# Kernel tuning notes

Hardware: AMD Instinct MI355X
Metric: run time of the kernel (lower is better)

Reference implementation:

```python
import jax, jax.numpy as jnp
import numpy as np

HIDDEN = 1024
Q_OUT = 2048
KV_OUT = 1024
HEAD_DIM = 128
N_Q = Q_OUT // HEAD_DIM      # 16
N_KV = KV_OUT // HEAD_DIM    # 8
EPS = 1e-6
ROPE_BASE = 10000.0


def _rms_norm(x, w, eps=EPS):
    # normalize over last dim (head_dim)
    ms = jnp.mean(x * x, axis=-1, keepdims=True)
    return x * jax.lax.rsqrt(ms + eps) * w


def _rope_cos_sin(t, dim=HEAD_DIM, base=ROPE_BASE):
    inv_freq = 1.0 / (base ** (jnp.arange(0, dim, 2, dtype=jnp.float32) / dim))
    pos = jnp.arange(t, dtype=jnp.float32)
    freqs = pos[:, None] * inv_freq[None, :]          # (T, D/2)
    emb = jnp.concatenate([freqs, freqs], axis=-1)    # (T, D)
    return jnp.cos(emb), jnp.sin(emb)


def _rotate_half(x):
    d = x.shape[-1] // 2
    return jnp.concatenate([-x[..., d:], x[..., :d]], axis=-1)


def setup_inputs() -> dict:
    key = jax.random.key(0)
    ks = jax.random.split(key, 7)
    def lin(k, fan_in, fan_out):
        # nn.Linear default init: U(-1/sqrt(fan_in), 1/sqrt(fan_in)); stored as (in, out) for x @ W
        bound = 1.0 / np.sqrt(fan_in)
        return jax.random.uniform(k, (fan_in, fan_out), jnp.float32, -bound, bound)
    return {
        "x": jax.random.normal(ks[0], (2, 2048, HIDDEN), jnp.float32),
        "Wq": lin(ks[1], HIDDEN, Q_OUT),
        "Wk": lin(ks[2], HIDDEN, KV_OUT),
        "Wv": lin(ks[3], HIDDEN, KV_OUT),
        "Wo": lin(ks[4], Q_OUT, HIDDEN),
        "q_norm_w": jnp.ones((HEAD_DIM,), jnp.float32),
        "k_norm_w": jnp.ones((HEAD_DIM,), jnp.float32),
    }


def reference(x, Wq, Wk, Wv, Wo, q_norm_w, k_norm_w):
    b, t, _ = x.shape
    # QKV projections, shaped to (B, H, T, D)
    q = (x @ Wq).reshape(b, t, N_Q, HEAD_DIM).transpose(0, 2, 1, 3)
    k = (x @ Wk).reshape(b, t, N_KV, HEAD_DIM).transpose(0, 2, 1, 3)
    v = (x @ Wv).reshape(b, t, N_KV, HEAD_DIM).transpose(0, 2, 1, 3)
    # per-head RMSNorm on q/k
    q = _rms_norm(q, q_norm_w)
    k = _rms_norm(k, k_norm_w)
    # RoPE (positions 0..T-1)
    cos, sin = _rope_cos_sin(t)                        # (T, D)
    cos = cos[None, None]; sin = sin[None, None]       # (1,1,T,D)
    q = q * cos + _rotate_half(q) * sin
    k = k * cos + _rotate_half(k) * sin
    # GQA: repeat_interleave kv heads to match q heads
    rep = N_Q // N_KV
    k_r = jnp.repeat(k, rep, axis=1)                   # (B, Hq, T, D)
    v_r = jnp.repeat(v, rep, axis=1)
    # causal attention
    scores = jnp.einsum('bhqd,bhkd->bhqk', q, k_r) / jnp.sqrt(jnp.asarray(HEAD_DIM, x.dtype))
    causal = jnp.triu(jnp.full((t, t), -jnp.inf, dtype=scores.dtype), k=1)[None, None]
    attn = jax.nn.softmax(scores + causal, axis=-1)
    out = jnp.einsum('bhqk,bhkd->bhqd', attn, v_r)     # (B, Hq, T, D)
    out = out.transpose(0, 2, 1, 3).reshape(b, t, Q_OUT)
    return out @ Wo
```

## Files before the change

kernel.cpp:

```cpp
#include <hip/hip_runtime.h>
#include <math.h>

typedef __attribute__((ext_vector_type(8))) short short8;
typedef __attribute__((ext_vector_type(4))) float f32x4;
typedef __attribute__((ext_vector_type(4))) unsigned int uint4v;

#define HIDDEN 1024
#define QOUT 2048
#define KVOUT 1024
#define HD 128
#define TSEQ 2048

__device__ __forceinline__ float bf2f(unsigned short h) {
    union { unsigned int u; float f; } x; x.u = ((unsigned int)h) << 16; return x.f;
}
__device__ __forceinline__ unsigned short f2bf(float f) {
    union { float f; unsigned int u; } x; x.f = f;
    unsigned int r = (x.u + 0x7fffu + ((x.u >> 16) & 1u)) >> 16;
    return (unsigned short)r;
}
__device__ __forceinline__ unsigned int pk2bf(float lo, float hi) {
    return (unsigned int)f2bf(lo) | ((unsigned int)f2bf(hi) << 16);
}

__device__ __forceinline__ void glds16(const unsigned short* g, unsigned short* l) {
    __builtin_amdgcn_global_load_lds(
        (const __attribute__((address_space(1))) unsigned int*)g,
        (__attribute__((address_space(3))) unsigned int*)l, 16, 0, 0);
}

__global__ __launch_bounds__(256) void prep(const float* __restrict__ x,
                                            const float* __restrict__ Wq,
                                            const float* __restrict__ Wk,
                                            const float* __restrict__ Wv,
                                            const float* __restrict__ Wo,
                                            unsigned short* __restrict__ xb,
                                            unsigned short* __restrict__ Wt,
                                            unsigned short* __restrict__ Wot) {
    int bid = blockIdx.x;
    int tid = threadIdx.x;
    if (bid < 4096) {
        int i = bid * 256 + tid;
        float4 v = *(const float4*)(x + (size_t)i * 4);
        unsigned short o[4] = {f2bf(v.x), f2bf(v.y), f2bf(v.z), f2bf(v.w)};
        *(unsigned long long*)(xb + (size_t)i * 4) = *(unsigned long long*)o;
        return;
    }
    bid -= 4096;
    const float* W; unsigned short* D; int K, N;
    if (bid < 512)       { W = Wq; D = Wt;                          K = 1024; N = 2048; }
    else if (bid < 768)  { bid -= 512;  W = Wk; D = Wt + (size_t)2048 * 1024; K = 1024; N = 1024; }
    else if (bid < 1024) { bid -= 768;  W = Wv; D = Wt + (size_t)3072 * 1024; K = 1024; N = 1024; }
    else                 { bid -= 1024; W = Wo; D = Wot;                      K = 2048; N = 1024; }
    __shared__ __attribute__((aligned(16))) unsigned short Ls[64 * 72];
    int ntiles = N >> 6;
    int kt = bid / ntiles, nt = bid - kt * ntiles;
    int k0 = kt * 64, n0 = nt * 64;
    for (int t = 0; t < 4; t++) {
        int idx = tid + t * 256;
        int r = idx >> 4, seg = idx & 15;
        float4 v = *(const float4*)(W + (size_t)(k0 + r) * N + n0 + seg * 4);
        int c = seg * 4;
        Ls[(c + 0) * 72 + r] = f2bf(v.x);
        Ls[(c + 1) * 72 + r] = f2bf(v.y);
        Ls[(c + 2) * 72 + r] = f2bf(v.z);
        Ls[(c + 3) * 72 + r] = f2bf(v.w);
    }
    __syncthreads();
    for (int t = 0; t < 2; t++) {
        int idx = tid + t * 256;
        int rr = idx >> 3, seg = idx & 7;
        uint4v v = *(const uint4v*)(Ls + rr * 72 + seg * 8);
        *(uint4v*)(D + (size_t)(n0 + rr) * K + k0 + seg * 8) = v;
    }
}

template <int OUT_BF16, int BN>
__global__ __launch_bounds__(256) void gemm_bt(const unsigned short* __restrict__ A,
                                               const unsigned short* __restrict__ Bt,
                                               void* __restrict__ Cout,
                                               int M, int N, int K) {
    constexpr int MT = (BN == 128) ? 4 : 2;
    __shared__ __attribute__((aligned(16))) unsigned short As[2][128 * 32];
    __shared__ __attribute__((aligned(16))) unsigned short Bs[2][BN * 32];
    const int tid = threadIdx.x;
    const int lane = tid & 63;
    const int warp = tid >> 6;
    const int ln = lane & 15;
    const int quad = lane >> 4;
    const int wm = (BN == 128) ? (warp >> 1) : warp;
    const int wn = (BN == 128) ? (warp & 1) : 0;
    const int m0 = blockIdx.y * 128;
    const int n0 = blockIdx.x * BN;

    const int srow = lane >> 2;
    const int schunk = (lane & 3) ^ (srow & 3);
    const unsigned short* Ag = A + (size_t)(m0 + warp * 16 + srow) * K + schunk * 8;
    const unsigned short* Bg = Bt + (size_t)(n0 + warp * 16 + srow) * K + schunk * 8;

    f32x4 acc[MT][4];
#pragma unroll
    for (int i = 0; i < MT; i++)
#pragma unroll
        for (int j = 0; j < 4; j++) acc[i][j] = (f32x4){0.f, 0.f, 0.f, 0.f};

    auto stage = [&](int k0, int bi) {
        glds16(Ag + k0, As[bi] + warp * 16 * 32);
        glds16(Ag + (size_t)64 * K + k0, As[bi] + warp * 16 * 32 + 64 * 32);
        glds16(Bg + k0, Bs[bi] + warp * 16 * 32);
        if (BN == 128) glds16(Bg + (size_t)64 * K + k0, Bs[bi] + warp * 16 * 32 + 64 * 32);
    };

    const int rq = quad ^ (ln & 3);
    const int KI = K >> 5;
    stage(0, 0);
    for (int it = 0; it < KI; it++) {
        __syncthreads();
        if (it + 1 < KI) stage((it + 1) << 5, (it + 1) & 1);
        const unsigned short* Ab = As[it & 1];
        const unsigned short* Bb = Bs[it & 1];
        short8 af[MT], bf[4];
#pragma unroll
        for (int mt = 0; mt < MT; mt++)
            af[mt] = *(const short8*)(Ab + (wm * (MT * 16) + mt * 16 + ln) * 32 + rq * 8);
#pragma unroll
        for (int nt = 0; nt < 4; nt++)
            bf[nt] = *(const short8*)(Bb + (wn * 64 + nt * 16 + ln) * 32 + rq * 8);
#pragma unroll
        for (int mt = 0; mt < MT; mt++)
#pragma unroll
            for (int nt = 0; nt < 4; nt++)
                acc[mt][nt] = __builtin_amdgcn_mfma_f32_16x16x32_bf16(bf[nt], af[mt], acc[mt][nt], 0, 0, 0);
    }
#pragma unroll
    for (int mt = 0; mt < MT; mt++) {
        int row = m0 + wm * (MT * 16) + mt * 16 + ln;
#pragma unroll
        for (int nt = 0; nt < 4; nt++) {
            int colb = n0 + wn * 64 + nt * 16 + quad * 4;
            if (OUT_BF16) {
                unsigned long long pk =
                    (unsigned long long)pk2bf(acc[mt][nt][0], acc[mt][nt][1]) |
                    ((unsigned long long)pk2bf(acc[mt][nt][2], acc[mt][nt][3]) << 32);
                *(unsigned long long*)((unsigned short*)Cout + (size_t)row * N + colb) = pk;
            } else {
                *(f32x4*)((float*)Cout + (size_t)row * N + colb) = acc[mt][nt];
            }
        }
    }
}

__global__ __launch_bounds__(256) void nrvt(const unsigned short* __restrict__ QKV,
                                            const float* __restrict__ qw,
                                            const float* __restrict__ kw,
                                            unsigned short* __restrict__ Q,
                                            unsigned short* __restrict__ Kb,
                                            unsigned short* __restrict__ Vt) {
    if (blockIdx.x < 24576) {
        int warp = threadIdx.x >> 6;
        int lane = threadIdx.x & 63;
        int gid = blockIdx.x * 4 + warp;
        int tok = gid / 24;
        int slot = gid - tok * 24;
        int b = tok >> 11, t = tok & 2047;
        const float* w;
        unsigned short* dst;
        int col0;
        if (slot < 16) {
            col0 = slot * HD;
            dst = Q + ((size_t)(b * 16 + slot) * TSEQ + t) * HD;
            w = qw;
        } else {
            int hk = slot - 16;
            col0 = QOUT + hk * HD;
            dst = Kb + ((size_t)(b * 8 + hk) * TSEQ + t) * HD;
            w = kw;
        }
        const unsigned short* row = QKV + (size_t)tok * 4096 + col0;
        float e0 = bf2f(row[lane]), e1 = bf2f(row[lane + 64]);
        float ss = e0 * e0 + e1 * e1;
        for (int off = 1; off < 64; off <<= 1) ss += __shfl_xor(ss, off);
        float rr = rsqrtf(ss * (1.0f / 128.0f) + 1e-6f);
        float n0 = e0 * rr * w[lane];
        float n1 = e1 * rr * w[lane + 64];
        float invf = __builtin_exp2f(-(float)lane * 0.20762050593045951f);
        float ang = (float)t * invf;
        float sf, cf;
        __sincosf(ang, &sf, &cf);
        dst[lane] = f2bf(n0 * cf - n1 * sf);
        dst[lane + 64] = f2bf(n1 * cf + n0 * sf);
        return;
    }
    __shared__ __attribute__((aligned(16))) unsigned short Ls[128 * 72];
    int bid = blockIdx.x - 24576;
    int tt = bid & 31, hk = (bid >> 5) & 7, b = bid >> 8;
    int t0 = tt * 64;
    int tid = threadIdx.x;
    const unsigned short* base = QKV + (size_t)(b * 2048 + t0) * 4096 + 3072 + hk * 128;
    for (int i = 0; i < 4; i++) {
        int idx = tid + i * 256;
        int r = idx >> 4, seg = idx & 15;
        uint4v v = *(const uint4v*)(base + (size_t)r * 4096 + seg * 8);
        unsigned short* pv = (unsigned short*)&v;
        int d = seg * 8;
        for (int jj = 0; jj < 8; jj++) Ls[(d + jj) * 72 + r] = pv[jj];
    }
    __syncthreads();
    unsigned short* out = Vt + (size_t)(b * 8 + hk) * 128 * 2048;
    for (int i = 0; i < 4; i++) {
        int idx = tid + i * 256;
        int d = idx >> 3, seg = idx & 7;
        uint4v v = *(const uint4v*)(Ls + d * 72 + seg * 8);
        *(uint4v*)(out + (size_t)d * 2048 + t0 + seg * 8) = v;
    }
}

__global__ __launch_bounds__(256, 2) void attn(const unsigned short* __restrict__ Q,
                                               const unsigned short* __restrict__ Kg,
                                               const unsigned short* __restrict__ Vt,
                                               unsigned short* __restrict__ Og) {
    __shared__ __attribute__((aligned(16))) unsigned short Ks[2][64 * 128];
    __shared__ __attribute__((aligned(16))) unsigned short Vs[2][128 * 64];
    __shared__ __attribute__((aligned(16))) unsigned short Ps[4][16 * 72];
    const int p = blockIdx.x;
    const int bh = blockIdx.y;
    const int b = bh >> 4, h = bh & 15, hk = h >> 1;
    const int tid = threadIdx.x;
    const int warp = tid >> 6, lane = tid & 63, ln = lane & 15, quad = lane >> 4;
    const int strip[2] = { p * 64 + warp * 16, (31 - p) * 64 + warp * 16 };
    const int jdiag[2] = { p, 31 - p };

    const unsigned short* Kbase = Kg + (size_t)(b * 8 + hk) * TSEQ * HD;
    const unsigned short* Vbase = Vt + (size_t)(b * 8 + hk) * HD * TSEQ;
    const unsigned short* Qh = Q + (size_t)(b * 16 + h) * TSEQ * HD;

    short8 qf[2][4];
#pragma unroll
    for (int st = 0; st < 2; st++)
#pragma unroll
        for (int kt = 0; kt < 4; kt++)
            qf[st][kt] = *(const short8*)(Qh + (size_t)(strip[st] + ln) * HD + kt * 32 + quad * 8);

    f32x4 o[2][8];
#pragma unroll
    for (int st = 0; st < 2; st++)
#pragma unroll
        for (int ot = 0; ot < 8; ot++) o[st][ot] = (f32x4){0.f, 0.f, 0.f, 0.f};
    float m_[2] = {-1e30f, -1e30f}, l_[2] = {0.f, 0.f};

    const int kr = lane >> 4;
    const int kc = lane & 15;
    const int vr = lane >> 3;
    const int vc = lane & 7;

    auto stage_kv = [&](int jt, int bi) {
        const int j0s = jt * 64;
        unsigned short* KsB = Ks[bi];
        unsigned short* VsB = Vs[bi];
#pragma unroll
        for (int c = 0; c < 4; c++) {
            int row = warp * 16 + c * 4 + kr;
            glds16(Kbase + (size_t)(j0s + row) * HD + ((kc ^ (row & 15)) * 8),
                   KsB + (warp * 16 + c * 4) * 128);
        }
#pragma unroll
        for (int c = 0; c < 4; c++) {
            int d = warp * 32 + c * 8 + vr;
            glds16(Vbase + (size_t)d * TSEQ + j0s + ((vc ^ (d & 7)) * 8),
                   VsB + (warp * 32 + c * 8) * 64);
        }
    };

    const float kscale = 0.12750580997495268f;
    const int nT = 32 - p;
    stage_kv(0, 0);
    for (int j = 0; j < nT; j++) {
        __syncthreads();
        if (j + 1 < nT) stage_kv(j + 1, (j + 1) & 1);
        const unsigned short* KsC = Ks[j & 1];
        const unsigned short* VsC = Vs[j & 1];
        const bool act0 = (j <= jdiag[0]);
        f32x4 s[2][4];
#pragma unroll
        for (int kb = 0; kb < 4; kb++) {
            s[0][kb] = (f32x4){0.f, 0.f, 0.f, 0.f};
            s[1][kb] = (f32x4){0.f, 0.f, 0.f, 0.f};
        }
#pragma unroll
        for (int kt = 0; kt < 4; kt++) {
            short8 kf[4];
#pragma unroll
            for (int kb = 0; kb < 4; kb++)
                kf[kb] = *(const short8*)(KsC + (kb * 16 + ln) * 128 + (((kt * 4 + quad) ^ ln) * 8));
#pragma unroll
            for (int kb = 0; kb < 4; kb++)
                s[1][kb] = __builtin_amdgcn_mfma_f32_16x16x32_bf16(kf[kb], qf[1][kt], s[1][kb], 0, 0, 0);
            if (act0)
#pragma unroll
                for (int kb = 0; kb < 4; kb++)
                    s[0][kb] = __builtin_amdgcn_mfma_f32_16x16x32_bf16(kf[kb], qf[0][kt], s[0][kb], 0, 0, 0);
        }
        short8 pf[2][2];
        float al[2] = {1.f, 1.f};
#pragma unroll
        for (int st = 0; st < 2; st++) {
            if (st == 0 && !act0) continue;
            float mx = -1e30f;
            if (j == jdiag[st]) {
                const int qloc = warp * 16 + ln;
#pragma unroll
                for (int kb = 0; kb < 4; kb++)
#pragma unroll
                    for (int r = 0; r < 4; r++) {
                        int kvloc = kb * 16 + quad * 4 + r;
                        float v = s[st][kb][r] * kscale;
                        v = (kvloc > qloc) ? -1e30f : v;
                        s[st][kb][r] = v;
                        mx = fmaxf(mx, v);
                    }
            } else {
#pragma unroll
                for (int kb = 0; kb < 4; kb++)
#pragma unroll
                    for (int r = 0; r < 4; r++) {
                        float v = s[st][kb][r] * kscale;
                        s[st][kb][r] = v;
                        mx = fmaxf(mx, v);
                    }
            }
            mx = fmaxf(mx, __shfl_xor(mx, 16));
            mx = fmaxf(mx, __shfl_xor(mx, 32));
            float mn = fmaxf(m_[st], mx);
            al[st] = __builtin_exp2f(m_[st] - mn);
            float sum = 0.f;
#pragma unroll
            for (int kb = 0; kb < 4; kb++)
#pragma unroll
                for (int r = 0; r < 4; r++) {
                    float pv = __builtin_exp2f(s[st][kb][r] - mn);
                    s[st][kb][r] = pv;
                    sum += pv;
                }
            sum += __shfl_xor(sum, 16);
            sum += __shfl_xor(sum, 32);
            m_[st] = mn;
            l_[st] = l_[st] * al[st] + sum;
#pragma unroll
            for (int kb = 0; kb < 4; kb++) {
                unsigned long long pk =
                    (unsigned long long)pk2bf(s[st][kb][0], s[st][kb][1]) |
                    ((unsigned long long)pk2bf(s[st][kb][2], s[st][kb][3]) << 32);
                *(unsigned long long*)(&Ps[warp][ln * 72 + kb * 16 + quad * 4]) = pk;
            }
            pf[st][0] = *(const short8*)(&Ps[warp][ln * 72 + quad * 8]);
            pf[st][1] = *(const short8*)(&Ps[warp][ln * 72 + 32 + quad * 8]);
        }
        if (act0 && __any(al[0] != 1.0f))
#pragma unroll
            for (int ot = 0; ot < 8; ot++)
#pragma unroll
                for (int r = 0; r < 4; r++) o[0][ot][r] *= al[0];
        if (__any(al[1] != 1.0f))
#pragma unroll
            for (int ot = 0; ot < 8; ot++)
#pragma unroll
                for (int r = 0; r < 4; r++) o[1][ot][r] *= al[1];
#pragma unroll
        for (int ot = 0; ot < 8; ot++) {
            short8 vf0 = *(const short8*)(VsC + (ot * 16 + ln) * 64 + ((quad ^ (ln & 7)) * 8));
            short8 vf1 = *(const short8*)(VsC + (ot * 16 + ln) * 64 + (((4 + quad) ^ (ln & 7)) * 8));
            o[1][ot] = __builtin_amdgcn_mfma_f32_16x16x32_bf16(vf0, pf[1][0], o[1][ot], 0, 0, 0);
            o[1][ot] = __builtin_amdgcn_mfma_f32_16x16x32_bf16(vf1, pf[1][1], o[1][ot], 0, 0, 0);
            if (act0) {
                o[0][ot] = __builtin_amdgcn_mfma_f32_16x16x32_bf16(vf0, pf[0][0], o[0][ot], 0, 0, 0);
                o[0][ot] = __builtin_amdgcn_mfma_f32_16x16x32_bf16(vf1, pf[0][1], o[0][ot], 0, 0, 0);
            }
        }
    }
#pragma unroll
    for (int st = 0; st < 2; st++) {
        float inv = 1.0f / l_[st];
        size_t rowoff = ((size_t)(b * TSEQ + strip[st] + ln)) * QOUT + h * 128 + quad * 4;
#pragma unroll
        for (int ot = 0; ot < 8; ot++) {
            unsigned long long pk =
                (unsigned long long)pk2bf(o[st][ot][0] * inv, o[st][ot][1] * inv) |
                ((unsigned long long)pk2bf(o[st][ot][2] * inv, o[st][ot][3] * inv) << 32);
            *(unsigned long long*)(Og + rowoff + ot * 16) = pk;
        }
    }
}

extern "C" void kernel_launch(void* const* d_in, const int* in_sizes, int n_in,
                              void* d_out, int out_size, void* d_ws, size_t ws_size,
                              hipStream_t stream) {
    (void)in_sizes; (void)n_in; (void)out_size;
    const float* x  = (const float*)d_in[0];
    const float* Wq = (const float*)d_in[1];
    const float* Wk = (const float*)d_in[2];
    const float* Wv = (const float*)d_in[3];
    const float* Wo = (const float*)d_in[4];
    const float* qw = (const float*)d_in[5];
    const float* kw = (const float*)d_in[6];

    char* ws = (char*)d_ws;
    const size_t MB = 1024 * 1024;
    unsigned short* Wt   = (unsigned short*)(ws);
    unsigned short* Wot  = (unsigned short*)(ws + 8 * MB);
    unsigned short* QKVb = (unsigned short*)(ws + 12 * MB);
    unsigned short* xb   = (unsigned short*)(ws + 44 * MB);
    unsigned short* Qb   = (unsigned short*)(ws + 52 * MB);
    unsigned short* Kb   = (unsigned short*)(ws + 68 * MB);
    unsigned short* Vtb  = (unsigned short*)(ws + 76 * MB);
    unsigned short* Ob   = (unsigned short*)(ws + 84 * MB);
    if (ws_size < 100 * MB) return;

    prep<<<dim3(5632), 256, 0, stream>>>(x, Wq, Wk, Wv, Wo, xb, Wt, Wot);
    gemm_bt<1, 128><<<dim3(32, 32), 256, 0, stream>>>(xb, Wt, QKVb, 4096, 4096, 1024);
    nrvt<<<dim3(25088), 256, 0, stream>>>(QKVb, qw, kw, Qb, Kb, Vtb);
    attn<<<dim3(16, 32), 256, 0, stream>>>(Qb, Kb, Vtb, Ob);
    gemm_bt<0, 64><<<dim3(16, 32), 256, 0, stream>>>(Ob, Wot, (float*)d_out, 4096, 1024, 2048);
}
```

Before: 286.2 us.

## Split paired-strip attention blocks into one strip per block with higher occupancy

The attention kernel no longer pairs a short and a long causal query strip in one block. It now launches one block per 64-row strip, twice as many blocks, with the longest strips scheduled first. The double-buffered K/V staging becomes a single buffer loaded between two barriers, the P-tile LDS round trip becomes cross-lane shuffles, and launch bounds rise to 4 blocks per CU. This trades explicit load/compute overlap within a block for more parallelism, higher occupancy and less register and LDS use, which risks exposing global-load latency and adding barrier cost.

Result: slower. 325.1 us (+13.6%).

```diff
diff --git a/kernel.cpp b/kernel.cpp
--- a/kernel.cpp
+++ b/kernel.cpp
@@ -10,6 +10,8 @@
 #define KVOUT 1024
 #define HD 128
 #define TSEQ 2048
+
+union U8 { uint4v u; short8 s; };
 
 __device__ __forceinline__ float bf2f(unsigned short h) {
     union { unsigned int u; float f; } x; x.u = ((unsigned int)h) << 16; return x.f;
@@ -215,179 +217,151 @@
     }
 }
 
-__global__ __launch_bounds__(256, 2) void attn(const unsigned short* __restrict__ Q,
+__global__ __launch_bounds__(256, 4) void attn(const unsigned short* __restrict__ Q,
                                                const unsigned short* __restrict__ Kg,
                                                const unsigned short* __restrict__ Vt,
                                                unsigned short* __restrict__ Og) {
-    __shared__ __attribute__((aligned(16))) unsigned short Ks[2][64 * 128];
-    __shared__ __attribute__((aligned(16))) unsigned short Vs[2][128 * 64];
-    __shared__ __attribute__((aligned(16))) unsigned short Ps[4][16 * 72];
-    const int p = blockIdx.x;
+    __shared__ __attribute__((aligned(16))) unsigned short Ks[64 * 128];
+    __shared__ __attribute__((aligned(16))) unsigned short Vs[128 * 64];
+    const int t = 31 - (int)blockIdx.x;
     const int bh = blockIdx.y;
     const int b = bh >> 4, h = bh & 15, hk = h >> 1;
     const int tid = threadIdx.x;
     const int warp = tid >> 6, lane = tid & 63, ln = lane & 15, quad = lane >> 4;
-    const int strip[2] = { p * 64 + warp * 16, (31 - p) * 64 + warp * 16 };
-    const int jdiag[2] = { p, 31 - p };
+    const int row0 = t * 64 + warp * 16;
 
     const unsigned short* Kbase = Kg + (size_t)(b * 8 + hk) * TSEQ * HD;
     const unsigned short* Vbase = Vt + (size_t)(b * 8 + hk) * HD * TSEQ;
     const unsigned short* Qh = Q + (size_t)(b * 16 + h) * TSEQ * HD;
 
-    short8 qf[2][4];
-#pragma unroll
-    for (int st = 0; st < 2; st++)
-#pragma unroll
-        for (int kt = 0; kt < 4; kt++)
-            qf[st][kt] = *(const short8*)(Qh + (size_t)(strip[st] + ln) * HD + kt * 32 + quad * 8);
-
-    f32x4 o[2][8];
-#pragma unroll
-    for (int st = 0; st < 2; st++)
-#pragma unroll
-        for (int ot = 0; ot < 8; ot++) o[st][ot] = (f32x4){0.f, 0.f, 0.f, 0.f};
-    float m_[2] = {-1e30f, -1e30f}, l_[2] = {0.f, 0.f};
+    short8 qf[4];
+#pragma unroll
+    for (int kt = 0; kt < 4; kt++)
+        qf[kt] = *(const short8*)(Qh + (size_t)(row0 + ln) * HD + kt * 32 + quad * 8);
+
+    f32x4 o[8];
+#pragma unroll
+    for (int ot = 0; ot < 8; ot++) o[ot] = (f32x4){0.f, 0.f, 0.f, 0.f};
+    float m_ = -1e30f, l_ = 0.f;
 
     const int kr = lane >> 4;
     const int kc = lane & 15;
     const int vr = lane >> 3;
     const int vc = lane & 7;
-
-    auto stage_kv = [&](int jt, int bi) {
-        const int j0s = jt * 64;
-        unsigned short* KsB = Ks[bi];
-        unsigned short* VsB = Vs[bi];
+    const int baseq = (quad & 1) * 2;
+    const int i0 = ln + 16 * baseq;
+    const int i1 = ln + 16 * (baseq + 1);
+    const bool qlow = quad < 2;
+
+    const float kscale = 0.12750580997495268f;
+    for (int j = 0; j <= t; j++) {
+        const int j0 = j * 64;
+        __syncthreads();
 #pragma unroll
         for (int c = 0; c < 4; c++) {
             int row = warp * 16 + c * 4 + kr;
-            glds16(Kbase + (size_t)(j0s + row) * HD + ((kc ^ (row & 15)) * 8),
-                   KsB + (warp * 16 + c * 4) * 128);
+            glds16(Kbase + (size_t)(j0 + row) * HD + ((kc ^ (row & 15)) * 8),
+                   Ks + (warp * 16 + c * 4) * 128);
         }
 #pragma unroll
         for (int c = 0; c < 4; c++) {
             int d = warp * 32 + c * 8 + vr;
-            glds16(Vbase + (size_t)d * TSEQ + j0s + ((vc ^ (d & 7)) * 8),
-                   VsB + (warp * 32 + c * 8) * 64);
-        }
-    };
-
-    const float kscale = 0.12750580997495268f;
-    const int nT = 32 - p;
-    stage_kv(0, 0);
-    for (int j = 0; j < nT; j++) {
+            glds16(Vbase + (size_t)d * TSEQ + j0 + ((vc ^ (d & 7)) * 8),
+                   Vs + (warp * 32 + c * 8) * 64);
+        }
         __syncthreads();
-        if (j + 1 < nT) stage_kv(j + 1, (j + 1) & 1);
-        const unsigned short* KsC = Ks[j & 1];
-        const unsigned short* VsC = Vs[j & 1];
-        const bool act0 = (j <= jdiag[0]);
-        f32x4 s[2][4];
-#pragma unroll
-        for (int kb = 0; kb < 4; kb++) {
-            s[0][kb] = (f32x4){0.f, 0.f, 0.f, 0.f};
-            s[1][kb] = (f32x4){0.f, 0.f, 0.f, 0.f};
-        }
+        f32x4 s[4];
+#pragma unroll
+        for (int kb = 0; kb < 4; kb++) s[kb] = (f32x4){0.f, 0.f, 0.f, 0.f};
 #pragma unroll
         for (int kt = 0; kt < 4; kt++) {
             short8 kf[4];
 #pragma unroll
             for (int kb = 0; kb < 4; kb++)
-                kf[kb] = *(const short8*)(KsC + (kb * 16 + ln) * 128 + (((kt * 4 + quad) ^ ln) * 8));
+                kf[kb] = *(const short8*)(Ks + (kb * 16 + ln) * 128 + (((kt * 4 + quad) ^ ln) * 8));
 #pragma unroll
             for (int kb = 0; kb < 4; kb++)
-                s[1][kb] = __builtin_amdgcn_mfma_f32_16x16x32_bf16(kf[kb], qf[1][kt], s[1][kb], 0, 0, 0);
-            if (act0)
-#pragma unroll
-                for (int kb = 0; kb < 4; kb++)
-                    s[0][kb] = __builtin_amdgcn_mfma_f32_16x16x32_bf16(kf[kb], qf[0][kt], s[0][kb], 0, 0, 0);
-        }
-        short8 pf[2][2];
-        float al[2] = {1.f, 1.f};
-#pragma unroll
-        for (int st = 0; st < 2; st++) {
-            if (st == 0 && !act0) continue;
-            float mx = -1e30f;
-            if (j == jdiag[st]) {
-                const int qloc = warp * 16 + ln;
-#pragma unroll
-                for (int kb = 0; kb < 4; kb++)
-#pragma unroll
-                    for (int r = 0; r < 4; r++) {
-                        int kvloc = kb * 16 + quad * 4 + r;
-                        float v = s[st][kb][r] * kscale;
-                        v = (kvloc > qloc) ? -1e30f : v;
-                        s[st][kb][r] = v;
-                        mx = fmaxf(mx, v);
-                    }
-            } else {
-#pragma unroll
-                for (int kb = 0; kb < 4; kb++)
-#pragma unroll
-                    for (int r = 0; r < 4; r++) {
-                        float v = s[st][kb][r] * kscale;
-                        s[st][kb][r] = v;
-                        mx = fmaxf(mx, v);
-                    }
+                s[kb] = __builtin_amdgcn_mfma_f32_16x16x32_bf16(kf[kb], qf[kt], s[kb], 0, 0, 0);
+        }
+        float mx = -1e30f;
+        if (j == t) {
+            const int qloc = warp * 16 + ln;
+#pragma unroll
+            for (int kb = 0; kb < 4; kb++)
+#pragma unroll
+                for (int r = 0; r < 4; r++) {
+                    int kvloc = kb * 16 + quad * 4 + r;
+                    float v = s[kb][r] * kscale;
+                    v = (kvloc > qloc) ? -1e30f : v;
+                    s[kb][r] = v;
+                    mx = fmaxf(mx, v);
+                }
+        } else {
+#pragma unroll
+            for (int kb = 0; kb < 4; kb++)
+#pragma unroll
+                for (int r = 0; r < 4; r++) {
+                    float v = s[kb][r] * kscale;
+                    s[kb][r] = v;
+                    mx = fmaxf(mx, v);
+                }
+        }
+        mx = fmaxf(mx, __shfl_xor(mx, 16));
+        mx = fmaxf(mx, __shfl_xor(mx, 32));
+        float mn = fmaxf(m_, mx);
+        float al = __builtin_exp2f(m_ - mn);
+        float sum = 0.f;
+#pragma unroll
+        for (int kb = 0; kb < 4; kb++)
+#pragma unroll
+            for (int r = 0; r < 4; r++) {
+                float pv = __builtin_exp2f(s[kb][r] - mn);
+                s[kb][r] = pv;
+                sum += pv;
             }
-            mx = fmaxf(mx, __shfl_xor(mx, 16));
-            mx = fmaxf(mx, __shfl_xor(mx, 32));
-            float mn = fmaxf(m_[st], mx);
-            al[st] = __builtin_exp2f(m_[st] - mn);
-            float sum = 0.f;
-#pragma unroll
-            for (int kb = 0; kb < 4; kb++)
-#pragma unroll
-                for (int r = 0; r < 4; r++) {
-                    float pv = __builtin_exp2f(s[st][kb][r] - mn);
-                    s[st][kb][r] = pv;
-                    sum += pv;
-                }
-            sum += __shfl_xor(sum, 16);
-            sum += __shfl_xor(sum, 32);
-            m_[st] = mn;
-            l_[st] = l_[st] * al[st] + sum;
-#pragma unroll
-            for (int kb = 0; kb < 4; kb++) {
-                unsigned long long pk =
-                    (unsigned long long)pk2bf(s[st][kb][0], s[st][kb][1]) |
-                    ((unsigned long long)pk2bf(s[st][kb][2], s[st][kb][3]) << 32);
-                *(unsigned long long*)(&Ps[warp][ln * 72 + kb * 16 + quad * 4]) = pk;
-            }
-            pf[st][0] = *(const short8*)(&Ps[warp][ln * 72 + quad * 8]);
-            pf[st][1] = *(const short8*)(&Ps[warp][ln * 72 + 32 + quad * 8]);
-        }
-        if (act0 && __any(al[0] != 1.0f))
+        sum += __shfl_xor(sum, 16);
+        sum += __shfl_xor(sum, 32);
+        m_ = mn;
+        l_ = l_ * al + sum;
+        unsigned int P2[4][2];
+#pragma unroll
+        for (int kb = 0; kb < 4; kb++) {
+            P2[kb][0] = pk2bf(s[kb][0], s[kb][1]);
+            P2[kb][1] = pk2bf(s[kb][2], s[kb][3]);
+        }
+        U8 pf0, pf1;
+        {
+            unsigned a, bb;
+            a = __shfl(P2[0][0], i0); bb = __shfl(P2[1][0], i0); pf0.u[0] = qlow ? a : bb;
+            a = __shfl(P2[0][1], i0); bb = __shfl(P2[1][1], i0); pf0.u[1] = qlow ? a : bb;
+            a = __shfl(P2[0][0], i1); bb = __shfl(P2[1][0], i1); pf0.u[2] = qlow ? a : bb;
+            a = __shfl(P2[0][1], i1); bb = __shfl(P2[1][1], i1); pf0.u[3] = qlow ? a : bb;
+            a = __shfl(P2[2][0], i0); bb = __shfl(P2[3][0], i0); pf1.u[0] = qlow ? a : bb;
+            a = __shfl(P2[2][1], i0); bb = __shfl(P2[3][1], i0); pf1.u[1] = qlow ? a : bb;
+            a = __shfl(P2[2][0], i1); bb = __shfl(P2[3][0], i1); pf1.u[2] = qlow ? a : bb;
+            a = __shfl(P2[2][1], i1); bb = __shfl(P2[3][1], i1); pf1.u[3] = qlow ? a : bb;
+        }
+        if (__any(al != 1.0f))
 #pragma unroll
             for (int ot = 0; ot < 8; ot++)
 #pragma unroll
-                for (int r = 0; r < 4; r++) o[0][ot][r] *= al[0];
-        if (__any(al[1] != 1.0f))
-#pragma unroll
-            for (int ot = 0; ot < 8; ot++)
-#pragma unroll
-                for (int r = 0; r < 4; r++) o[1][ot][r] *= al[1];
+                for (int r = 0; r < 4; r++) o[ot][r] *= al;
 #pragma unroll
         for (int ot = 0; ot < 8; ot++) {
-            short8 vf0 = *(const short8*)(VsC + (ot * 16 + ln) * 64 + ((quad ^ (ln & 7)) * 8));
-            short8 vf1 = *(const short8*)(VsC + (ot * 16 + ln) * 64 + (((4 + quad) ^ (ln & 7)) * 8));
-            o[1][ot] = __builtin_amdgcn_mfma_f32_16x16x32_bf16(vf0, pf[1][0], o[1][ot], 0, 0, 0);
-            o[1][ot] = __builtin_amdgcn_mfma_f32_16x16x32_bf16(vf1, pf[1][1], o[1][ot], 0, 0, 0);
-            if (act0) {
-                o[0][ot] = __builtin_amdgcn_mfma_f32_16x16x32_bf16(vf0, pf[0][0], o[0][ot], 0, 0, 0);
-                o[0][ot] = __builtin_amdgcn_mfma_f32_16x16x32_bf16(vf1, pf[0][1], o[0][ot], 0, 0, 0);
-            }
-        }
-    }
-#pragma unroll
-    for (int st = 0; st < 2; st++) {
-        float inv = 1.0f / l_[st];
-        size_t rowoff = ((size_t)(b * TSEQ + strip[st] + ln)) * QOUT + h * 128 + quad * 4;
-#pragma unroll
-        for (int ot = 0; ot < 8; ot++) {
-            unsigned long long pk =
-                (unsigned long long)pk2bf(o[st][ot][0] * inv, o[st][ot][1] * inv) |
-                ((unsigned long long)pk2bf(o[st][ot][2] * inv, o[st][ot][3] * inv) << 32);
-            *(unsigned long long*)(Og + rowoff + ot * 16) = pk;
-        }
+            short8 vf0 = *(const short8*)(Vs + (ot * 16 + ln) * 64 + ((quad ^ (ln & 7)) * 8));
+            short8 vf1 = *(const short8*)(Vs + (ot * 16 + ln) * 64 + (((4 + quad) ^ (ln & 7)) * 8));
+            o[ot] = __builtin_amdgcn_mfma_f32_16x16x32_bf16(vf0, pf0.s, o[ot], 0, 0, 0);
+            o[ot] = __builtin_amdgcn_mfma_f32_16x16x32_bf16(vf1, pf1.s, o[ot], 0, 0, 0);
+        }
+    }
+    float inv = 1.0f / l_;
+    size_t rowoff = ((size_t)(b * TSEQ + row0 + ln)) * QOUT + h * 128 + quad * 4;
+#pragma unroll
+    for (int ot = 0; ot < 8; ot++) {
+        unsigned long long pk =
+            (unsigned long long)pk2bf(o[ot][0] * inv, o[ot][1] * inv) |
+            ((unsigned long long)pk2bf(o[ot][2] * inv, o[ot][3] * inv) << 32);
+        *(unsigned long long*)(Og + rowoff + ot * 16) = pk;
     }
 }
 
@@ -418,6 +392,6 @@
     prep<<<dim3(5632), 256, 0, stream>>>(x, Wq, Wk, Wv, Wo, xb, Wt, Wot);
     gemm_bt<1, 128><<<dim3(32, 32), 256, 0, stream>>>(xb, Wt, QKVb, 4096, 4096, 1024);
     nrvt<<<dim3(25088), 256, 0, stream>>>(QKVb, qw, kw, Qb, Kb, Vtb);
-    attn<<<dim3(16, 32), 256, 0, stream>>>(Qb, Kb, Vtb, Ob);
+    attn<<<dim3(32, 32), 256, 0, stream>>>(Qb, Kb, Vtb, Ob);
     gemm_bt<0, 64><<<dim3(16, 32), 256, 0, stream>>>(Ob, Wot, (float*)d_out, 4096, 1024, 2048);
 }
```
